# Performance work log

Hardware: AMD Instinct MI355X
Metric: run time of the kernel (lower is better)

The kernel has to match this reference:

```python
import jax, jax.numpy as jnp
import numpy as np

H = 1024      # hidden_dim
V = 50257     # vocab_size
E = 512       # embedding_dim
PAD = 0       # padding_idx
B = 128       # batch
S = 512       # src_len


def setup_inputs() -> dict:
    key = jax.random.key(0)
    ks = jax.random.split(key, 16)
    sc = 0.02
    emb_table = jax.random.normal(ks[0], (V, E), jnp.float32) * sc
    emb_table = emb_table.at[PAD].set(0.0)  # padding_idx row is zero
    return {
        "decoder_input": jax.random.randint(ks[1], (B,), 0, V),
        "decoder_hidden": jax.random.normal(ks[2], (1, B, H), jnp.float32),
        "encoder_outputs": jax.random.normal(ks[3], (B, S, 2 * H), jnp.float32),
        "emb_table": emb_table,
        "W_ah": jax.random.normal(ks[4], (H, H), jnp.float32) * sc,
        "b_ah": jnp.zeros((H,), jnp.float32),
        "W_ae": jax.random.normal(ks[5], (H, 2 * H), jnp.float32) * sc,
        "b_ae": jnp.zeros((H,), jnp.float32),
        "w_score": jax.random.normal(ks[6], (H,), jnp.float32) * sc,
        "W_ih": jax.random.normal(ks[7], (3 * H, E + 2 * H), jnp.float32) * sc,
        "W_hh": jax.random.normal(ks[8], (3 * H, H), jnp.float32) * sc,
        "b_ih": jnp.zeros((3 * H,), jnp.float32),
        "b_hh": jnp.zeros((3 * H,), jnp.float32),
        "W_out": jax.random.normal(ks[9], (V, H), jnp.float32) * sc,
        "b_out": jnp.zeros((V,), jnp.float32),
    }


def reference(decoder_input, decoder_hidden, encoder_outputs, emb_table,
              W_ah, b_ah, W_ae, b_ae, w_score, W_ih, W_hh, b_ih, b_hh,
              W_out, b_out):
    h = decoder_hidden[0]                                  # [B,H]
    emb = emb_table[decoder_input]                         # [B,E]

    # Bahdanau attention
    ah = h @ W_ah.T + b_ah                                 # [B,H]
    ae = jnp.einsum('bsd,hd->bsh', encoder_outputs, W_ae) + b_ae  # [B,S,H]
    scores = jnp.tanh(ah[:, None, :] + ae) @ w_score       # [B,S]
    attn = jax.nn.softmax(scores, axis=1)                  # [B,S]
    ctx = jnp.einsum('bs,bsd->bd', attn, encoder_outputs)  # [B,2H]

    # GRU single step (PyTorch gate layout: r, z, n)
    x = jnp.concatenate([emb, ctx], axis=1)                # [B,E+2H]
    gx = x @ W_ih.T + b_ih                                 # [B,3H]
    gh = h @ W_hh.T + b_hh                                 # [B,3H]
    r = jax.nn.sigmoid(gx[:, :H] + gh[:, :H])
    z = jax.nn.sigmoid(gx[:, H:2 * H] + gh[:, H:2 * H])
    n = jnp.tanh(gx[:, 2 * H:] + r * gh[:, 2 * H:])
    h_new = (1.0 - z) * n + z * h                          # [B,H]

    out = h_new @ W_out.T + b_out                          # [B,V]
    return out[:, None, :], h_new[None]                    # [B,1,V], [1,B,H]
```

## Files before the change

### kernel.cpp

```cpp
#include <hip/hip_runtime.h>
#include <hip/hip_bf16.h>

#define DEVI __device__ __forceinline__

typedef short bf16x8 __attribute__((ext_vector_type(8)));
typedef float f32x4  __attribute__((ext_vector_type(4)));

static constexpr int Bb   = 128;
static constexpr int Ss   = 512;
static constexpr int Hh   = 1024;
static constexpr int Ee   = 512;
static constexpr int Vv   = 50257;
static constexpr int TWOH = 2048;

DEVI short f2bf(float f){ __hip_bfloat16 h = __float2bfloat16(f); return *reinterpret_cast<short*>(&h); }
DEVI float bf2f(short s){ __hip_bfloat16 h = *reinterpret_cast<__hip_bfloat16*>(&s); return __bfloat162float(h); }

DEVI float tanh_fast(float x){
  float e = __expf(2.0f*x);
  return 1.0f - 2.0f/(e + 1.0f);
}

DEVI bf16x8 pack8(f32x4 a, f32x4 b){
  bf16x8 v;
  v[0]=f2bf(a[0]); v[1]=f2bf(a[1]); v[2]=f2bf(a[2]); v[3]=f2bf(a[3]);
  v[4]=f2bf(b[0]); v[5]=f2bf(b[1]); v[6]=f2bf(b[2]); v[7]=f2bf(b[3]);
  return v;
}

DEVI void gld_lds16(const void* g, void* l){
  __builtin_amdgcn_global_load_lds((const __attribute__((address_space(1))) void*)g,
                                   (__attribute__((address_space(3))) void*)l, 16, 0, 0);
}

DEVI f32x4 mfma16(bf16x8 a, bf16x8 b, f32x4 c){
  return __builtin_amdgcn_mfma_f32_16x16x32_bf16(a, b, c, 0, 0, 0);
}

__global__ void k_prep(const float* __restrict__ wae, short* __restrict__ waeb,
                       const float* __restrict__ h, short* __restrict__ hb,
                       const int* __restrict__ dec_in, const float* __restrict__ emb,
                       short* __restrict__ xb)
{
  const int total_wae = Hh*TWOH;
  const int total_h   = Bb*Hh;
  const int total_emb = Bb*Ee;
  const int total = total_wae + total_h + total_emb;
  for (int i = blockIdx.x*blockDim.x + threadIdx.x; i < total; i += gridDim.x*blockDim.x){
    if (i < total_wae) waeb[i] = f2bf(wae[i]);
    else if (i < total_wae + total_h){ int j = i - total_wae; hb[j] = f2bf(h[j]); }
    else {
      int j = i - total_wae - total_h;
      int b = j >> 9, e = j & 511;
      xb[b*2560 + e] = f2bf(emb[(size_t)dec_in[b]*Ee + e]);
    }
  }
}

__launch_bounds__(512)
__global__ void k_scores_fuse(const float* __restrict__ enc, short* __restrict__ encb,
                              const short* __restrict__ waeb,
                              const float* __restrict__ ahb, const float* __restrict__ b_ah,
                              const float* __restrict__ b_ae, const float* __restrict__ wsc,
                              float* __restrict__ scores)
{
  __shared__ __align__(16) char LDSB[131072];
  const int q  = blockIdx.x;
  const int xcd = q & 7, sl = q >> 3;
  const int rt = xcd*32 + (sl>>2), nb = sl & 3;
  const int tid = threadIdx.x, wid = tid>>6, lane = tid&63;
  const int wr = wid>>2, wc = wid&3;
  const int srow = lane>>3, l7 = lane&7;
  const int lo = lane&15, hi4 = lane>>4;
  const int swk = (l7 ^ srow)*8;

  const float* Ag = enc  + (size_t)rt*256*TWOH + (size_t)(wid*8+srow)*TWOH + swk;
  const short* Bg = waeb + (size_t)nb*256*TWOH + (size_t)(wid*8+srow)*TWOH + swk;
  short*       Eg = encb + (size_t)rt*256*TWOH + (size_t)(wid*8+srow)*TWOH + swk;
  const bool we = (nb == 0) && (encb != nullptr);

  char* AWc = LDSB + wid*1024 + lane*16;
  char* BW  = LDSB + 65536 + wid*1024;
  const char* AR = LDSB + (wr*128 + lo)*128;
  const char* BR = LDSB + 65536 + (wc*64 + lo)*128;
  const int sw0 = (hi4*16) ^ (l7<<4);
  const int sw1 = (64 + hi4*16) ^ (l7<<4);

  f32x4 acc[8][4] = {};
  f32x4 pa[4][2];

  auto STB = [&](int buf, int kt){
    #pragma unroll
    for (int rnd=0; rnd<4; ++rnd)
      gld_lds16(Bg + (size_t)rnd*64*TWOH + kt*64, BW + buf*32768 + rnd*8192);
  };
  auto PREFA = [&](int kt){
    #pragma unroll
    for (int rnd=0; rnd<4; ++rnd){
      const float* p = Ag + (size_t)rnd*64*TWOH + kt*64;
      pa[rnd][0] = *(const f32x4*)p; pa[rnd][1] = *(const f32x4*)(p+4);
    }
  };
  auto COMMITA = [&](int buf){
    #pragma unroll
    for (int rnd=0; rnd<4; ++rnd)
      *(bf16x8*)(AWc + buf*32768 + rnd*8192) = pack8(pa[rnd][0], pa[rnd][1]);
  };
  auto STOREE = [&](int kt){
    #pragma unroll
    for (int rnd=0; rnd<4; ++rnd)
      *(bf16x8*)(Eg + (size_t)rnd*64*TWOH + kt*64) = pack8(pa[rnd][0], pa[rnd][1]);
  };

  STB(0,0);
  PREFA(0); COMMITA(0);
  if (we) STOREE(0);
  PREFA(1);
  asm volatile("s_waitcnt lgkmcnt(0)" ::: "memory");
  __builtin_amdgcn_s_barrier();
  __builtin_amdgcn_sched_barrier(0);

  for (int t = 0; t < 32; ++t){
    const int cur = t&1, nxt = cur^1;
    const int aO = cur*32768, bO = cur*32768;
    bf16x8 af[4], bq[4];

    if (t<31){ STB(nxt, t+1); PREFA(t+1); }
    __builtin_amdgcn_sched_barrier(0);

    #pragma unroll
    for (int j=0;j<4;++j) bq[j] = *(const bf16x8*)(BR + bO + j*2048 + sw0);
    #pragma unroll
    for (int i=0;i<4;++i) af[i] = *(const bf16x8*)(AR + aO + i*2048 + sw0);
    __builtin_amdgcn_s_setprio(1);
    #pragma unroll
    for (int i=0;i<4;++i)
      #pragma unroll
      for (int j=0;j<4;++j)
        acc[i][j] = mfma16(af[i], bq[j], acc[i][j]);
    __builtin_amdgcn_s_setprio(0);
    #pragma unroll
    for (int i=0;i<4;++i) af[i] = *(const bf16x8*)(AR + aO + (4+i)*2048 + sw0);
    __builtin_amdgcn_s_setprio(1);
    #pragma unroll
    for (int i=0;i<4;++i)
      #pragma unroll
      for (int j=0;j<4;++j)
        acc[4+i][j] = mfma16(af[i], bq[j], acc[4+i][j]);
    __builtin_amdgcn_s_setprio(0);

    #pragma unroll
    for (int j=0;j<4;++j) bq[j] = *(const bf16x8*)(BR + bO + j*2048 + sw1);
    #pragma unroll
    for (int i=0;i<4;++i) af[i] = *(const bf16x8*)(AR + aO + i*2048 + sw1);
    __builtin_amdgcn_s_setprio(1);
    #pragma unroll
    for (int i=0;i<4;++i)
      #pragma unroll
      for (int j=0;j<4;++j)
        acc[i][j] = mfma16(af[i], bq[j], acc[i][j]);
    __builtin_amdgcn_s_setprio(0);
    #pragma unroll
    for (int i=0;i<4;++i) af[i] = *(const bf16x8*)(AR + aO + (4+i)*2048 + sw1);
    __builtin_amdgcn_s_setprio(1);
    #pragma unroll
    for (int i=0;i<4;++i)
      #pragma unroll
      for (int j=0;j<4;++j)
        acc[4+i][j] = mfma16(af[i], bq[j], acc[4+i][j]);
    __builtin_amdgcn_s_setprio(0);

    __builtin_amdgcn_sched_barrier(0);
    if (t<31){
      COMMITA(nxt);
      if (we) STOREE(t+1);
    }
    asm volatile("s_waitcnt lgkmcnt(0)" ::: "memory");
    __builtin_amdgcn_s_barrier();
    __builtin_amdgcn_sched_barrier(0);
  }
  const int b = rt >> 1;
  float w4[4], t4[4];
  #pragma unroll
  for (int j=0;j<4;++j){
    int n = nb*256 + wc*64 + j*16 + lo;
    w4[j] = wsc[n];
    t4[j] = ahb[b*Hh + n] + b_ah[n] + b_ae[n];
  }
  #pragma unroll
  for (int i=0;i<8;++i){
    #pragma unroll
    for (int q2=0;q2<4;++q2){
      int m = rt*256 + wr*128 + i*16 + hi4*4 + q2;
      float s = 0.f;
      #pragma unroll
      for (int j=0;j<4;++j) s += tanh_fast(t4[j] + acc[i][j][q2]) * w4[j];
      s += __shfl_xor(s,1); s += __shfl_xor(s,2); s += __shfl_xor(s,4); s += __shfl_xor(s,8);
      if (lo == 0) atomicAdd(&scores[m], s);
    }
  }
}

template<int MODE>
__launch_bounds__(256)
__global__ void k_gemm128(const short* __restrict__ A, int lda,
                          const float* __restrict__ B0, const float* __restrict__ B1,
                          float* __restrict__ O0, float* __restrict__ O1,
                          const float* __restrict__ bias, int kiters)
{
  __shared__ __align__(16) short As[2][128*64];
  __shared__ __align__(16) short Bs[2][128*64];
  const int nb = blockIdx.x;
  const int tid = threadIdx.x, wid = tid>>6, lane = tid&63;
  const int wr = wid>>1, wc = wid&1;
  const int srow = lane>>3, l7 = lane&7;
  const int swk = (l7 ^ srow) * 8;

  const float* Bt; int noff; float* Ot; int ostride;
  if constexpr (MODE==0){
    if (nb < 8){ Bt = B0; noff = 0;    Ot = O0; ostride = Hh;   }
    else       { Bt = B1; noff = 1024; Ot = O1; ostride = 3*Hh; }
  } else if constexpr (MODE==1){ Bt = B0; noff = 0; Ot = O0; ostride = 3*Hh; }
  else { Bt = B0; noff = 0; Ot = O0; ostride = Vv; }

  f32x4 acc[4][4] = {};
  f32x4 pb0[4], pb1[4];

  auto stageA = [&](int s, int kt){
    #pragma unroll
    for (int i=0;i<4;++i){
      int c = wid*4+i, row = c*8+srow;
      gld_lds16(A + (size_t)row*lda + kt*64 + swk, (char*)As[s] + c*1024);
    }
  };
  auto prefB = [&](int kt){
    #pragma unroll
    for (int i=0;i<4;++i){
      int row = (wid*4+i)*8+srow;
      int n = nb*128 + row - noff;
      if constexpr (MODE==2) n = (n > Vv-1) ? (Vv-1) : n;
      const float* bp = Bt + (size_t)n*lda + kt*64 + l7*8;
      pb0[i] = *(const f32x4*)bp; pb1[i] = *(const f32x4*)(bp+4);
    }
  };
  auto commitB = [&](int s){
    #pragma unroll
    for (int i=0;i<4;++i){
      int row = (wid*4+i)*8+srow;
      *(bf16x8*)((char*)Bs[s] + row*128 + ((l7^srow)<<4)) = pack8(pb0[i], pb1[i]);
    }
  };

  const int kt0 = blockIdx.y * kiters, kend = kt0 + kiters;
  stageA(0, kt0); prefB(kt0); commitB(0);
  __syncthreads();

  int cur = 0;
  for (int kt = kt0; kt < kend; ++kt){
    if (kt+1 < kend){ stageA(cur^1, kt+1); prefB(kt+1); }
    #pragma unroll
    for (int kk=0;kk<2;++kk){
      bf16x8 af[4], bq[4];
      const int sw = (kk*64 + (lane>>4)*16) ^ (l7<<4);
      #pragma unroll
      for (int i=0;i<4;++i) af[i] = *(const bf16x8*)((const char*)As[cur] + (wr*64+i*16+(lane&15))*128 + sw);
      #pragma unroll
      for (int j=0;j<4;++j) bq[j] = *(const bf16x8*)((const char*)Bs[cur] + (wc*64+j*16+(lane&15))*128 + sw);
      #pragma unroll
      for (int i=0;i<4;++i)
        #pragma unroll
        for (int j=0;j<4;++j)
          acc[i][j] = mfma16(af[i], bq[j], acc[i][j]);
    }
    if (kt+1 < kend) commitB(cur^1);
    __syncthreads();
    cur ^= 1;
  }
  const int lo = lane&15, hi = lane>>4;
  #pragma unroll
  for (int i=0;i<4;++i){
    #pragma unroll
    for (int j=0;j<4;++j){
      int n = nb*128 + wc*64 + j*16 + lo - noff;
      #pragma unroll
      for (int q=0;q<4;++q){
        int m = wr*64 + i*16 + hi*4 + q;
        float v = acc[i][j][q];
        if constexpr (MODE==2){
          if (n < Vv) O0[(size_t)m*Vv + n] = v + bias[n];
        } else {
          atomicAdd(&Ot[(size_t)m*ostride + n], v);
        }
      }
    }
  }
}

__global__ void k_softmax(const float* __restrict__ scores, float* __restrict__ attn)
{
  __shared__ float red[512];
  const int b = blockIdx.x, tid = threadIdx.x;
  float v = scores[b*Ss + tid];
  red[tid] = v; __syncthreads();
  for (int off=256; off>0; off>>=1){ if (tid<off) red[tid] = fmaxf(red[tid], red[tid+off]); __syncthreads(); }
  float mx = red[0]; __syncthreads();
  float e = __expf(v - mx);
  red[tid] = e; __syncthreads();
  for (int off=256; off>0; off>>=1){ if (tid<off) red[tid] += red[tid+off]; __syncthreads(); }
  attn[b*Ss + tid] = e / red[0];
}

__global__ void k_ctx_bf16(const short* __restrict__ encb, const float* __restrict__ attn,
                           float* __restrict__ ctxp)
{
  __shared__ float a[128];
  const int bid = blockIdx.x, b = bid>>2, ch = bid&3, tid = threadIdx.x;
  if (tid < 128) a[tid] = attn[b*Ss + ch*128 + tid];
  __syncthreads();
  const short* e0 = encb + (size_t)(b*Ss + ch*128)*TWOH + tid*8;
  float s[8] = {};
  for (int r=0; r<128; ++r){
    bf16x8 v = *(const bf16x8*)(e0 + (size_t)r*TWOH);
    float w = a[r];
    #pragma unroll
    for (int j=0;j<8;++j) s[j] += w * bf2f(v[j]);
  }
  float* o = ctxp + (size_t)ch*Bb*TWOH + (size_t)b*TWOH + tid*8;
  #pragma unroll
  for (int j=0;j<8;++j) o[j] = s[j];
}

__global__ void k_ctxfin(const float* __restrict__ ctxp, short* __restrict__ xb)
{
  const int g = blockIdx.x*256 + threadIdx.x;
  const int b = g >> 11, col = g & 2047;
  const int N = Bb*TWOH;
  float v = ctxp[g] + ctxp[N+g] + ctxp[2*N+g] + ctxp[3*N+g];
  xb[b*2560 + 512 + col] = f2bf(v);
}

__global__ void k_ctx_f32(const float* __restrict__ enc, const float* __restrict__ attn,
                          short* __restrict__ xb)
{
  __shared__ float a[512];
  const int ch = blockIdx.x, b = blockIdx.y, tid = threadIdx.x;
  a[tid]     = attn[b*Ss + tid];
  a[tid+256] = attn[b*Ss + tid + 256];
  __syncthreads();
  const float* e0 = enc + (size_t)b*Ss*TWOH + ch*256 + tid;
  float s0=0.f, s1=0.f, s2=0.f, s3=0.f;
  for (int s=0; s<512; s+=4){
    s0 += a[s]   * e0[(size_t)(s  )*TWOH];
    s1 += a[s+1] * e0[(size_t)(s+1)*TWOH];
    s2 += a[s+2] * e0[(size_t)(s+2)*TWOH];
    s3 += a[s+3] * e0[(size_t)(s+3)*TWOH];
  }
  xb[b*2560 + 512 + ch*256 + tid] = f2bf(s0+s1+s2+s3);
}

__global__ void k_gates(const float* __restrict__ gx, const float* __restrict__ gh,
                        const float* __restrict__ b_ih, const float* __restrict__ b_hh,
                        const float* __restrict__ h, float* __restrict__ hnew_out,
                        short* __restrict__ hnewb)
{
  const int gid = blockIdx.x*256 + threadIdx.x;
  const int b = gid >> 10, j = gid & 1023;
  float xr = gx[b*3072 + j]        + b_ih[j];
  float xz = gx[b*3072 + 1024 + j] + b_ih[1024+j];
  float xn = gx[b*3072 + 2048 + j] + b_ih[2048+j];
  float hr = gh[b*3072 + j]        + b_hh[j];
  float hz = gh[b*3072 + 1024 + j] + b_hh[1024+j];
  float hn = gh[b*3072 + 2048 + j] + b_hh[2048+j];
  float r = 1.f/(1.f + __expf(-(xr+hr)));
  float z = 1.f/(1.f + __expf(-(xz+hz)));
  float n = tanhf(xn + r*hn);
  float hv = (1.f - z)*n + z*h[b*Hh + j];
  hnew_out[gid] = hv;
  hnewb[gid] = f2bf(hv);
}

extern "C" void kernel_launch(void* const* d_in, const int* in_sizes, int n_in,
                              void* d_out, int out_size, void* d_ws, size_t ws_size,
                              hipStream_t stream)
{
  const int*   dec   = (const int*)  d_in[0];
  const float* h     = (const float*)d_in[1];
  const float* enc   = (const float*)d_in[2];
  const float* emb   = (const float*)d_in[3];
  const float* W_ah  = (const float*)d_in[4];
  const float* b_ah  = (const float*)d_in[5];
  const float* W_ae  = (const float*)d_in[6];
  const float* b_ae  = (const float*)d_in[7];
  const float* wsc   = (const float*)d_in[8];
  const float* W_ih  = (const float*)d_in[9];
  const float* W_hh  = (const float*)d_in[10];
  const float* b_ih  = (const float*)d_in[11];
  const float* b_hh  = (const float*)d_in[12];
  const float* W_out = (const float*)d_in[13];
  const float* b_out = (const float*)d_in[14];
  float* out = (float*)d_out;
  float* hnew_out = out + (size_t)Bb*Vv;

  char* w = (char*)d_ws;
  float* scores = (float*)w;  w += (size_t)65536*4;
  float* ahb    = (float*)w;  w += (size_t)131072*4;
  float* ghb    = (float*)w;  w += (size_t)393216*4;
  float* gxb    = (float*)w;  w += (size_t)393216*4;
  size_t zero_bytes = (size_t)(w - (char*)d_ws);
  float* attn   = (float*)w;  w += (size_t)65536*4;
  short* waeb   = (short*)w;  w += (size_t)2097152*2;
  short* xb     = (short*)w;  w += (size_t)128*2560*2;
  short* hb     = (short*)w;  w += (size_t)131072*2;
  short* hnb    = (short*)w;  w += (size_t)131072*2;
  float* ctxp   = (float*)w;  w += (size_t)4*Bb*TWOH*4;
  short* encb   = (short*)w;  w += (size_t)65536*2048*2;
  const bool big = ((size_t)(w - (char*)d_ws) <= ws_size);

  hipMemsetAsync(d_ws, 0, zero_bytes, stream);
  k_prep<<<4096, 256, 0, stream>>>(W_ae, waeb, h, hb, dec, emb, xb);
  k_gemm128<0><<<dim3(32,2), 256, 0, stream>>>(hb, 1024, W_ah, W_hh, ahb, ghb, nullptr, 8);
  k_scores_fuse<<<1024, 512, 0, stream>>>(enc, big ? encb : nullptr, waeb,
                                          ahb, b_ah, b_ae, wsc, scores);
  k_softmax<<<128, 512, 0, stream>>>(scores, attn);
  if (big){
    k_ctx_bf16<<<512, 256, 0, stream>>>(encb, attn, ctxp);
    k_ctxfin<<<1024, 256, 0, stream>>>(ctxp, xb);
  } else {
    k_ctx_f32<<<dim3(8,128), 256, 0, stream>>>(enc, attn, xb);
  }
  k_gemm128<1><<<dim3(24,4), 256, 0, stream>>>(xb, 2560, W_ih, nullptr, gxb, nullptr, nullptr, 10);
  k_gates<<<512, 256, 0, stream>>>(gxb, ghb, b_ih, b_hh, h, hnew_out, hnb);
  k_gemm128<2><<<dim3(393,1), 256, 0, stream>>>(hnb, 1024, W_out, nullptr, out, nullptr, b_out, 16);
}
```

Baseline: 531.8 us.

## Halve scores GEMM M-tile and single-buffer A with register prefetch

The fused attention-score GEMM now uses 128-row A tiles instead of 256 and launches twice as many blocks. The A tile moves to a single LDS buffer fed by a two-iteration-ahead register prefetch with explicit vmcnt waits and an extra barrier. LDS use drops from 128 KB to 80 KB and accumulators halve, which is meant to raise occupancy and hide global latency. In exchange each block reuses the W_ae tile over fewer rows, so W_ae traffic doubles, and each k-step now needs an extra barrier.

```diff
diff --git a/kernel.cpp b/kernel.cpp
--- a/kernel.cpp
+++ b/kernel.cpp
@@ -57,37 +57,37 @@
   }
 }
 
-__launch_bounds__(512)
+__launch_bounds__(512, 4)
 __global__ void k_scores_fuse(const float* __restrict__ enc, short* __restrict__ encb,
                               const short* __restrict__ waeb,
                               const float* __restrict__ ahb, const float* __restrict__ b_ah,
                               const float* __restrict__ b_ae, const float* __restrict__ wsc,
                               float* __restrict__ scores)
 {
-  __shared__ __align__(16) char LDSB[131072];
+  __shared__ __align__(16) char LDSB[81920];
   const int q  = blockIdx.x;
   const int xcd = q & 7, sl = q >> 3;
-  const int rt = xcd*32 + (sl>>2), nb = sl & 3;
+  const int rt = xcd*64 + (sl>>2), nb = sl & 3;
   const int tid = threadIdx.x, wid = tid>>6, lane = tid&63;
   const int wr = wid>>2, wc = wid&3;
   const int srow = lane>>3, l7 = lane&7;
   const int lo = lane&15, hi4 = lane>>4;
   const int swk = (l7 ^ srow)*8;
 
-  const float* Ag = enc  + (size_t)rt*256*TWOH + (size_t)(wid*8+srow)*TWOH + swk;
+  const float* Ag = enc  + (size_t)rt*128*TWOH + (size_t)(wid*8+srow)*TWOH + swk;
   const short* Bg = waeb + (size_t)nb*256*TWOH + (size_t)(wid*8+srow)*TWOH + swk;
-  short*       Eg = encb + (size_t)rt*256*TWOH + (size_t)(wid*8+srow)*TWOH + swk;
+  short*       Eg = encb + (size_t)rt*128*TWOH + (size_t)(wid*8+srow)*TWOH + swk;
   const bool we = (nb == 0) && (encb != nullptr);
 
   char* AWc = LDSB + wid*1024 + lane*16;
-  char* BW  = LDSB + 65536 + wid*1024;
-  const char* AR = LDSB + (wr*128 + lo)*128;
-  const char* BR = LDSB + 65536 + (wc*64 + lo)*128;
+  char* BW  = LDSB + 16384 + wid*1024;
+  const char* AR = LDSB + (wr*64 + lo)*128;
+  const char* BR = LDSB + 16384 + (wc*64 + lo)*128;
   const int sw0 = (hi4*16) ^ (l7<<4);
   const int sw1 = (64 + hi4*16) ^ (l7<<4);
 
-  f32x4 acc[8][4] = {};
-  f32x4 pa[4][2];
+  f32x4 acc[4][4] = {};
+  f32x4 pa[2][2];
 
   auto STB = [&](int buf, int kt){
     #pragma unroll
@@ -96,24 +96,24 @@
   };
   auto PREFA = [&](int kt){
     #pragma unroll
-    for (int rnd=0; rnd<4; ++rnd){
+    for (int rnd=0; rnd<2; ++rnd){
       const float* p = Ag + (size_t)rnd*64*TWOH + kt*64;
       pa[rnd][0] = *(const f32x4*)p; pa[rnd][1] = *(const f32x4*)(p+4);
     }
   };
-  auto COMMITA = [&](int buf){
-    #pragma unroll
-    for (int rnd=0; rnd<4; ++rnd)
-      *(bf16x8*)(AWc + buf*32768 + rnd*8192) = pack8(pa[rnd][0], pa[rnd][1]);
+  auto COMMITA = [&](){
+    #pragma unroll
+    for (int rnd=0; rnd<2; ++rnd)
+      *(bf16x8*)(AWc + rnd*8192) = pack8(pa[rnd][0], pa[rnd][1]);
   };
   auto STOREE = [&](int kt){
     #pragma unroll
-    for (int rnd=0; rnd<4; ++rnd)
+    for (int rnd=0; rnd<2; ++rnd)
       *(bf16x8*)(Eg + (size_t)rnd*64*TWOH + kt*64) = pack8(pa[rnd][0], pa[rnd][1]);
   };
 
   STB(0,0);
-  PREFA(0); COMMITA(0);
+  PREFA(0); COMMITA();
   if (we) STOREE(0);
   PREFA(1);
   asm volatile("s_waitcnt lgkmcnt(0)" ::: "memory");
@@ -121,17 +121,16 @@
   __builtin_amdgcn_sched_barrier(0);
 
   for (int t = 0; t < 32; ++t){
-    const int cur = t&1, nxt = cur^1;
-    const int aO = cur*32768, bO = cur*32768;
+    const int bO = (t&1)*32768;
     bf16x8 af[4], bq[4];
 
-    if (t<31){ STB(nxt, t+1); PREFA(t+1); }
+    if (t<31) STB((t+1)&1, t+1);
     __builtin_amdgcn_sched_barrier(0);
 
     #pragma unroll
     for (int j=0;j<4;++j) bq[j] = *(const bf16x8*)(BR + bO + j*2048 + sw0);
     #pragma unroll
-    for (int i=0;i<4;++i) af[i] = *(const bf16x8*)(AR + aO + i*2048 + sw0);
+    for (int i=0;i<4;++i) af[i] = *(const bf16x8*)(AR + i*2048 + sw0);
     __builtin_amdgcn_s_setprio(1);
     #pragma unroll
     for (int i=0;i<4;++i)
@@ -140,19 +139,9 @@
         acc[i][j] = mfma16(af[i], bq[j], acc[i][j]);
     __builtin_amdgcn_s_setprio(0);
     #pragma unroll
-    for (int i=0;i<4;++i) af[i] = *(const bf16x8*)(AR + aO + (4+i)*2048 + sw0);
-    __builtin_amdgcn_s_setprio(1);
-    #pragma unroll
-    for (int i=0;i<4;++i)
-      #pragma unroll
-      for (int j=0;j<4;++j)
-        acc[4+i][j] = mfma16(af[i], bq[j], acc[4+i][j]);
-    __builtin_amdgcn_s_setprio(0);
-
-    #pragma unroll
     for (int j=0;j<4;++j) bq[j] = *(const bf16x8*)(BR + bO + j*2048 + sw1);
     #pragma unroll
-    for (int i=0;i<4;++i) af[i] = *(const bf16x8*)(AR + aO + i*2048 + sw1);
+    for (int i=0;i<4;++i) af[i] = *(const bf16x8*)(AR + i*2048 + sw1);
     __builtin_amdgcn_s_setprio(1);
     #pragma unroll
     for (int i=0;i<4;++i)
@@ -160,26 +149,22 @@
       for (int j=0;j<4;++j)
         acc[i][j] = mfma16(af[i], bq[j], acc[i][j]);
     __builtin_amdgcn_s_setprio(0);
-    #pragma unroll
-    for (int i=0;i<4;++i) af[i] = *(const bf16x8*)(AR + aO + (4+i)*2048 + sw1);
-    __builtin_amdgcn_s_setprio(1);
-    #pragma unroll
-    for (int i=0;i<4;++i)
-      #pragma unroll
-      for (int j=0;j<4;++j)
-        acc[4+i][j] = mfma16(af[i], bq[j], acc[4+i][j]);
-    __builtin_amdgcn_s_setprio(0);
-
+
+    __builtin_amdgcn_s_barrier();
     __builtin_amdgcn_sched_barrier(0);
+
     if (t<31){
-      COMMITA(nxt);
+      COMMITA();
       if (we) STOREE(t+1);
-    }
+      if (t<30) PREFA(t+2);
+    }
+    if (t<30)       asm volatile("s_waitcnt vmcnt(8)" ::: "memory");
+    else if (t==30) asm volatile("s_waitcnt vmcnt(0)" ::: "memory");
     asm volatile("s_waitcnt lgkmcnt(0)" ::: "memory");
     __builtin_amdgcn_s_barrier();
     __builtin_amdgcn_sched_barrier(0);
   }
-  const int b = rt >> 1;
+  const int b = rt >> 2;
   float w4[4], t4[4];
   #pragma unroll
   for (int j=0;j<4;++j){
@@ -188,10 +173,10 @@
     t4[j] = ahb[b*Hh + n] + b_ah[n] + b_ae[n];
   }
   #pragma unroll
-  for (int i=0;i<8;++i){
+  for (int i=0;i<4;++i){
     #pragma unroll
     for (int q2=0;q2<4;++q2){
-      int m = rt*256 + wr*128 + i*16 + hi4*4 + q2;
+      int m = rt*128 + wr*64 + i*16 + hi4*4 + q2;
       float s = 0.f;
       #pragma unroll
       for (int j=0;j<4;++j) s += tanh_fast(t4[j] + acc[i][j][q2]) * w4[j];
@@ -419,7 +404,7 @@
   hipMemsetAsync(d_ws, 0, zero_bytes, stream);
   k_prep<<<4096, 256, 0, stream>>>(W_ae, waeb, h, hb, dec, emb, xb);
   k_gemm128<0><<<dim3(32,2), 256, 0, stream>>>(hb, 1024, W_ah, W_hh, ahb, ghb, nullptr, 8);
-  k_scores_fuse<<<1024, 512, 0, stream>>>(enc, big ? encb : nullptr, waeb,
+  k_scores_fuse<<<2048, 512, 0, stream>>>(enc, big ? encb : nullptr, waeb,
                                           ahb, b_ah, b_ae, wsc, scores);
   k_softmax<<<128, 512, 0, stream>>>(scores, attn);
   if (big){
```

After: 577.9 us. +8.7%, slower.
